# Optimization experiments

Hardware: AMD Instinct MI355X
Metric: run time of the kernel (lower is better)

Reference implementation:

```python
import jax, jax.numpy as jnp
import numpy as np

TEMPERATURE = 0.07


def setup_inputs() -> dict:
    B, NB_PER, K, M, D = 32, 128, 8, 4, 256  # batches, bsl1k per batch, dict targets per batch, embeds per target, feat dim
    key = jax.random.key(0)
    kb, kd = jax.random.split(key)
    feats_bsl1k = jax.random.normal(kb, (B * NB_PER, D), dtype=jnp.float32)
    feats_dict = jax.random.normal(kd, (B * K * M, D), dtype=jnp.float32)
    # dict side: per batch, K distinct targets (first one is the mouthing word), M embeddings each
    batch_dict = np.repeat(np.arange(B), K * M).astype(np.int32)
    targets_dict = np.repeat(np.arange(B * K), M).astype(np.int32)  # sorted, distinct across batches
    one_mouth = np.concatenate([np.ones(1, np.int32), np.zeros(K - 1, np.int32)])
    is_mouthing_dict = np.tile(np.repeat(one_mouth, M), B).astype(np.int32)
    # bsl1k side: half the clips carry the batch's mouthing target, half are background (-1)
    batch_bsl1k = np.repeat(np.arange(B), NB_PER).astype(np.int32)
    tb = np.full((B, NB_PER), -1, dtype=np.int32)
    tb[:, : NB_PER // 2] = (np.arange(B, dtype=np.int32) * K)[:, None]
    targets_bsl1k = tb.reshape(-1)
    unique_targets = np.arange(B * K, dtype=np.int32)  # == unique_consecutive(targets_dict)
    return {
        "feats_bsl1k": feats_bsl1k,
        "feats_dict": feats_dict,
        "targets_bsl1k": jnp.asarray(targets_bsl1k),
        "targets_dict": jnp.asarray(targets_dict),
        "batch_bsl1k": jnp.asarray(batch_bsl1k),
        "batch_dict": jnp.asarray(batch_dict),
        "is_mouthing_dict": jnp.asarray(is_mouthing_dict),
        "unique_targets": jnp.asarray(unique_targets),
        "n_batches": B,
    }


def _loss(feats_bsl1k, feats_dict, targets_bsl1k, targets_dict, batch_bsl1k,
          batch_dict, is_mouthing_dict, unique_targets, n_batches):
    G = unique_targets.shape[0]
    fb = feats_bsl1k / jnp.linalg.norm(feats_bsl1k, axis=1, keepdims=True)
    fd = feats_dict / jnp.linalg.norm(feats_dict, axis=1, keepdims=True)
    dist = (fb @ fd.T) / TEMPERATURE  # [Nb, Nd]

    # group index of each dict embedding (unique_targets is sorted)
    g_idx = jnp.searchsorted(unique_targets, targets_dict).astype(jnp.int32)  # [Nd]
    # per-batch mouthing word (exactly one per batch, mirrors .item() in torch)
    mouth_word = jax.ops.segment_max(
        jnp.where(is_mouthing_dict == 1, targets_dict, -1), batch_dict, num_segments=n_batches)
    group_batch = jax.ops.segment_max(batch_dict, g_idx, num_segments=G)
    group_is_mouth = jax.ops.segment_max(is_mouthing_dict, g_idx, num_segments=G)

    # match[i, g]: bsl1k embedding i matches dict target group g (== match_multi collapsed per target)
    is_fg = targets_bsl1k != -1
    mw = mouth_word[batch_bsl1k]  # [Nb]
    match = jnp.where(
        is_fg[:, None],
        unique_targets[None, :] == mw[:, None],
        (group_batch[None, :] == batch_bsl1k[:, None]) & (group_is_mouth[None, :] == 0),
    )  # [Nb, G] bool

    # diff_batch_match: matched pairs from different batches are excluded from the denominator
    DB = match[:, g_idx] & (batch_bsl1k[:, None] != batch_dict[None, :])  # [Nb, Nd]

    c = jax.lax.stop_gradient(jnp.max(dist))  # shared lse shift; cancels in den - num
    E = jnp.exp(dist - c)                     # raw pair weights (numerator)
    A = jnp.where(DB, 0.0, E)                 # denominator weights with cross-batch matches removed
    matchf = match.astype(dist.dtype)

    Ecg = jax.ops.segment_sum(E.T, g_idx, num_segments=G)  # [G, Nb] column-group sums
    Acg = jax.ops.segment_sum(A.T, g_idx, num_segments=G)  # [G, Nb]

    # numerator[g] = lse over cross product {matched bsl1k rows} x {group-g dict cols}
    num_sum = jnp.einsum('gi,ig->g', Ecg, matchf)
    # denominator[g] = lse over union (group cols OR matched rows) minus cross-batch matches,
    # via inclusion-exclusion: cols + rows - intersection
    t1 = jax.ops.segment_sum(A.sum(0), g_idx, num_segments=G)
    t2 = jnp.einsum('ig,i->g', matchf, A.sum(1))
    t3 = jnp.einsum('gi,ig->g', Acg, matchf)
    den_sum = t1 + t2 - t3
    return jnp.mean(jnp.log(den_sum) - jnp.log(num_sum))


def reference(feats_bsl1k, feats_dict, targets_bsl1k, targets_dict, batch_bsl1k,
              batch_dict, is_mouthing_dict, unique_targets, n_batches):
    return _loss(feats_bsl1k, feats_dict, targets_bsl1k, targets_dict, batch_bsl1k,
                 batch_dict, is_mouthing_dict, unique_targets, n_batches)
```

## Files before the change

kernel.cpp:

```cpp
#include <hip/hip_runtime.h>
#include <math.h>

#define INVT (1.0f / 0.07f)
#define CSHIFT (1.0f / 0.07f)

using bf16x8 = __attribute__((ext_vector_type(8))) short;
using f32x4  = __attribute__((ext_vector_type(4))) float;

__device__ __forceinline__ int lower_bound_i(const int* a, int n, int v) {
    int lo = 0, hi = n;
    while (lo < hi) { int mid = (lo + hi) >> 1; if (a[mid] < v) lo = mid + 1; else hi = mid; }
    return lo;
}

__device__ __forceinline__ unsigned short f2bf(float x) {
    unsigned int u = __float_as_uint(x);
    unsigned int r = (u + 0x7fffu + ((u >> 16) & 1u)) >> 16;
    return (unsigned short)r;
}

__device__ __forceinline__ float agent_ld(const float* p) {
    return __hip_atomic_load(p, __ATOMIC_RELAXED, __HIP_MEMORY_SCOPE_AGENT);
}
__device__ __forceinline__ void agent_st(float* p, float v) {
    __hip_atomic_store(p, v, __ATOMIC_RELAXED, __HIP_MEMORY_SCOPE_AGENT);
}

__global__ __launch_bounds__(256)
void k_prep(const float* __restrict__ fb, const float* __restrict__ fd,
            int Nb, int Nd, int D,
            unsigned short* __restrict__ fbt, unsigned short* __restrict__ fdt,
            unsigned int* __restrict__ zbase, int zcount,
            const int* __restrict__ td, const int* __restrict__ bd,
            const int* __restrict__ im,
            int* __restrict__ mouth_word) {
    __shared__ __align__(16) unsigned short lbuf[32 * 256];
    int t = threadIdx.x;

    int nthreads = gridDim.x * blockDim.x;
    for (int zi = blockIdx.x * blockDim.x + t; zi < zcount; zi += nthreads) zbase[zi] = 0u;

    if (blockIdx.x == 0) {
        for (int i = t; i < Nb; i += blockDim.x) mouth_word[i] = -1;
        __syncthreads();
        for (int j = t; j < Nd; j += blockDim.x) {
            if (im[j] == 1) atomicMax(&mouth_word[bd[j]], td[j]);
        }
    }

    int R0 = blockIdx.x * 32;
    if (R0 >= Nb + Nd) return;
    const float* src; unsigned short* dst; int rt0;
    if (R0 < Nb) { src = fb + (size_t)R0 * D; dst = fbt; rt0 = R0 >> 4; }
    else         { src = fd + (size_t)(R0 - Nb) * D; dst = fdt; rt0 = (R0 - Nb) >> 4; }

    int row = t >> 3, kp = t & 7;
    const float* rp = src + (size_t)row * D;
    float4 v[8];
    float ss = 0.f;
    #pragma unroll
    for (int i = 0; i < 8; ++i) {
        v[i] = *(const float4*)(rp + 4 * (kp + 8 * i));
        ss += v[i].x * v[i].x + v[i].y * v[i].y + v[i].z * v[i].z + v[i].w * v[i].w;
    }
    ss += __shfl_xor(ss, 1, 64);
    ss += __shfl_xor(ss, 2, 64);
    ss += __shfl_xor(ss, 4, 64);
    float inv = rsqrtf(ss);
    #pragma unroll
    for (int i = 0; i < 8; ++i) {
        ushort4 o;
        o.x = f2bf(v[i].x * inv); o.y = f2bf(v[i].y * inv);
        o.z = f2bf(v[i].z * inv); o.w = f2bf(v[i].w * inv);
        *(ushort4*)&lbuf[row * 256 + 4 * (kp + 8 * i)] = o;
    }
    __syncthreads();

    int ktiles = D >> 5;
    #pragma unroll
    for (int j = 0; j < 4; ++j) {
        int c = t + 256 * j;
        int tile = c >> 6, l = c & 63;
        int rtl = tile >> 3, kt = tile & 7;
        int srow = rtl * 16 + (l & 15), sk = kt * 32 + (l >> 4) * 8;
        ulonglong2 d = *(const ulonglong2*)&lbuf[srow * 256 + sk];
        *(ulonglong2*)(dst + (((size_t)((rt0 + rtl) * ktiles + kt)) << 9) + l * 8) = d;
    }
}

__global__ __launch_bounds__(256, 4)
void k_main(const unsigned short* __restrict__ fbt, const unsigned short* __restrict__ fdt,
            const int* __restrict__ tb, const int* __restrict__ bb_arr,
            const int* __restrict__ td, const int* __restrict__ bd,
            const int* __restrict__ im, const int* __restrict__ ut,
            const int* __restrict__ mouth_word,
            int Nb, int Nd, int D, int G,
            float* __restrict__ rowpart, float* __restrict__ colpart,
            float* __restrict__ mnum, float* __restrict__ m1, float* __restrict__ m3,
            float* __restrict__ t2g, float* __restrict__ bgs,
            unsigned int* __restrict__ rowcnt, unsigned int* __restrict__ colcnt,
            unsigned int* __restrict__ dcnt, float* __restrict__ out) {
    __shared__ float cnum[64], ct1[64], ct3[64], rsum[64];
    __shared__ int rowflag, colflag, lastflag;

    int t = threadIdx.x, lane = t & 63, wid = t >> 6;
    int wr = wid >> 1, wc = wid & 1;
    int bm = blockIdx.x * 64, bn = blockIdx.y * 64;
    int l15 = lane & 15, lhi = lane >> 4;

    if (t < 64) { cnum[t] = 0.f; ct1[t] = 0.f; ct3[t] = 0.f; rsum[t] = 0.f; }

    int ktiles = D >> 5;
    const unsigned short* a0p = fbt + (((size_t)(((bm >> 4) + wr * 2) * ktiles)) << 9) + lane * 8;
    const unsigned short* a1p = a0p + ((size_t)ktiles << 9);
    const unsigned short* b0p = fdt + (((size_t)(((bn >> 4) + wc * 2) * ktiles)) << 9) + lane * 8;
    const unsigned short* b1p = b0p + ((size_t)ktiles << 9);

    f32x4 acc[2][2] = {};
    bf16x8 ca0 = *(const bf16x8*)a0p;
    bf16x8 ca1 = *(const bf16x8*)a1p;
    bf16x8 cb0 = *(const bf16x8*)b0p;
    bf16x8 cb1 = *(const bf16x8*)b1p;
    size_t o = 0;
    #pragma unroll 7
    for (int kt = 0; kt + 1 < ktiles; ++kt) {
        o += 512;
        bf16x8 na0 = *(const bf16x8*)(a0p + o);
        bf16x8 na1 = *(const bf16x8*)(a1p + o);
        bf16x8 nb0 = *(const bf16x8*)(b0p + o);
        bf16x8 nb1 = *(const bf16x8*)(b1p + o);
        acc[0][0] = __builtin_amdgcn_mfma_f32_16x16x32_bf16(ca0, cb0, acc[0][0], 0, 0, 0);
        acc[0][1] = __builtin_amdgcn_mfma_f32_16x16x32_bf16(ca0, cb1, acc[0][1], 0, 0, 0);
        acc[1][0] = __builtin_amdgcn_mfma_f32_16x16x32_bf16(ca1, cb0, acc[1][0], 0, 0, 0);
        acc[1][1] = __builtin_amdgcn_mfma_f32_16x16x32_bf16(ca1, cb1, acc[1][1], 0, 0, 0);
        ca0 = na0; ca1 = na1; cb0 = nb0; cb1 = nb1;
    }
    acc[0][0] = __builtin_amdgcn_mfma_f32_16x16x32_bf16(ca0, cb0, acc[0][0], 0, 0, 0);
    acc[0][1] = __builtin_amdgcn_mfma_f32_16x16x32_bf16(ca0, cb1, acc[0][1], 0, 0, 0);
    acc[1][0] = __builtin_amdgcn_mfma_f32_16x16x32_bf16(ca1, cb0, acc[1][0], 0, 0, 0);
    acc[1][1] = __builtin_amdgcn_mfma_f32_16x16x32_bf16(ca1, cb1, acc[1][1], 0, 0, 0);

    int cgb[2], cgm[2], cgc[2];
    #pragma unroll
    for (int nj = 0; nj < 2; ++nj) {
        int col = bn + wc * 32 + nj * 16 + l15;
        cgb[nj] = bd[col]; cgm[nj] = im[col]; cgc[nj] = td[col];
    }

    float pnum[2] = {0.f, 0.f}, pt1[2] = {0.f, 0.f}, pt3[2] = {0.f, 0.f};
    float prow[2][4];

    #pragma unroll
    for (int mi = 0; mi < 2; ++mi) {
        #pragma unroll
        for (int r = 0; r < 4; ++r) {
            int i = bm + wr * 32 + mi * 16 + lhi * 4 + r;
            int tbi = tb[i], bbi = bb_arr[i];
            int mw = mouth_word[bbi];
            bool fg = (tbi != -1);
            float pr = 0.f;
            #pragma unroll
            for (int nj = 0; nj < 2; ++nj) {
                float e = __expf(acc[mi][nj][r] * INVT - CSHIFT);
                bool match = fg ? (cgc[nj] == mw) : ((cgb[nj] == bbi) && (cgm[nj] == 0));
                float a = (match && (bbi != cgb[nj])) ? 0.f : e;
                pnum[nj] += match ? e : 0.f;
                pt1[nj] += a;
                pt3[nj] += match ? a : 0.f;
                pr += a;
            }
            prow[mi][r] = pr;
        }
    }

    __syncthreads();

    #pragma unroll
    for (int nj = 0; nj < 2; ++nj) {
        float n = pnum[nj], x1 = pt1[nj], x3 = pt3[nj];
        n  += __shfl_xor(n, 16, 64);  n  += __shfl_xor(n, 32, 64);
        x1 += __shfl_xor(x1, 16, 64); x1 += __shfl_xor(x1, 32, 64);
        x3 += __shfl_xor(x3, 16, 64); x3 += __shfl_xor(x3, 32, 64);
        if (lhi == 0) {
            int c = wc * 32 + nj * 16 + l15;
            atomicAdd(&cnum[c], n); atomicAdd(&ct1[c], x1); atomicAdd(&ct3[c], x3);
        }
    }
    #pragma unroll
    for (int mi = 0; mi < 2; ++mi) {
        #pragma unroll
        for (int r = 0; r < 4; ++r) {
            float v = prow[mi][r];
            v += __shfl_xor(v, 1, 64); v += __shfl_xor(v, 2, 64);
            v += __shfl_xor(v, 4, 64); v += __shfl_xor(v, 8, 64);
            if (l15 == 0) atomicAdd(&rsum[wr * 32 + mi * 16 + lhi * 4 + r], v);
        }
    }
    __syncthreads();

    float* cp = colpart + (size_t)(blockIdx.x & 7) * 3 * Nd;
    if (t < 64) {
        atomicAdd(&cp[bn + t], cnum[t]);
        atomicAdd(&cp[Nd + bn + t], ct1[t]);
        atomicAdd(&cp[2 * Nd + bn + t], ct3[t]);
    } else if (t < 128) {
        atomicAdd(&rowpart[(size_t)(blockIdx.y & 3) * Nb + bm + (t - 64)], rsum[t - 64]);
    }

    asm volatile("s_waitcnt vmcnt(0)" ::: "memory");
    __syncthreads();
    if (t == 0) {
        rowflag = (atomicAdd(&rowcnt[blockIdx.x * 16], 1u) == gridDim.y - 1) ? 1 : 0;
        colflag = (atomicAdd(&colcnt[blockIdx.y * 16], 1u) == gridDim.x - 1) ? 1 : 0;
    }
    __syncthreads();
    int nfin = rowflag + colflag;
    if (nfin == 0) return;

    if (rowflag && t < 64) {
        int i = bm + t;
        float r = agent_ld(&rowpart[i]) + agent_ld(&rowpart[Nb + i])
                + agent_ld(&rowpart[2 * Nb + i]) + agent_ld(&rowpart[3 * Nb + i]);
        int tbi = tb[i], bbi = bb_arr[i] & 1023;
        if (tbi != -1) {
            int g = lower_bound_i(ut, G, mouth_word[bbi]);
            atomicAdd(&t2g[g], r);
        } else {
            atomicAdd(&bgs[bbi], r);
        }
    }
    if (colflag && t < 192) {
        int c = t / 3, arr = t - c * 3;
        int col = bn + c;
        float s0 = 0.f;
        #pragma unroll
        for (int p = 0; p < 8; ++p)
            s0 += agent_ld(&colpart[(size_t)p * 3 * Nd + (size_t)arr * Nd + col]);
        float* dst = (arr == 0 ? mnum : (arr == 1 ? m1 : m3)) + col;
        agent_st(dst, s0);
    }

    asm volatile("s_waitcnt vmcnt(0)" ::: "memory");
    __syncthreads();
    if (t == 0) {
        unsigned int newv = atomicAdd(dcnt, (unsigned int)nfin) + (unsigned int)nfin;
        lastflag = (newv == gridDim.x + gridDim.y) ? 1 : 0;
    }
    __syncthreads();
    if (!lastflag) return;

    __shared__ float red[256];
    float acc2 = 0.f;
    for (int g = t; g < G; g += 256) {
        int s = lower_bound_i(td, Nd, ut[g]);
        int e = (g + 1 < G) ? lower_bound_i(td, Nd, ut[g + 1]) : Nd;
        float sn = 0.f, s1 = 0.f, s3 = 0.f;
        for (int c = s; c < e; ++c) {
            sn += agent_ld(&mnum[c]);
            s1 += agent_ld(&m1[c]);
            s3 += agent_ld(&m3[c]);
        }
        int gb = bd[s], gm = im[s];
        float t2 = agent_ld(&t2g[g]);
        if (gm == 0 && gb >= 0 && gb < 1024) t2 += agent_ld(&bgs[gb]);
        acc2 += logf(s1 + t2 - s3) - logf(sn);
    }
    red[t] = acc2;
    __syncthreads();
    for (int k = 128; k >= 1; k >>= 1) {
        if (t < k) red[t] += red[t + k];
        __syncthreads();
    }
    if (t == 0) out[0] = red[0] / (float)G;
}

extern "C" void kernel_launch(void* const* d_in, const int* in_sizes, int n_in,
                              void* d_out, int out_size, void* d_ws, size_t ws_size,
                              hipStream_t stream) {
    const float* fb = (const float*)d_in[0];
    const float* fd = (const float*)d_in[1];
    const int* tb = (const int*)d_in[2];
    const int* td = (const int*)d_in[3];
    const int* bb = (const int*)d_in[4];
    const int* bd = (const int*)d_in[5];
    const int* im = (const int*)d_in[6];
    const int* ut = (const int*)d_in[7];

    int Nb = in_sizes[2];
    int Nd = in_sizes[3];
    int G  = in_sizes[7];
    int D  = in_sizes[0] / Nb;
    float* out = (float*)d_out;

    char* p = (char*)d_ws;
    unsigned short* fbt = (unsigned short*)p; p += (size_t)Nb * D * sizeof(unsigned short);
    unsigned short* fdt = (unsigned short*)p; p += (size_t)Nd * D * sizeof(unsigned short);
    char* zstart = p;
    float* rowpart = (float*)p;  p += (size_t)4 * Nb * sizeof(float);
    float* colpart = (float*)p;  p += (size_t)24 * Nd * sizeof(float);
    float* t2g = (float*)p;      p += 1024 * sizeof(float);
    float* bgs = (float*)p;      p += 1024 * sizeof(float);
    unsigned int* rowcnt = (unsigned int*)p; p += 64 * 16 * sizeof(unsigned int);
    unsigned int* colcnt = (unsigned int*)p; p += 16 * 16 * sizeof(unsigned int);
    unsigned int* dcnt = (unsigned int*)p;   p += 16 * sizeof(unsigned int);
    int zcount = (int)((p - zstart) / 4);
    float* mnum = (float*)p; p += (size_t)Nd * sizeof(float);
    float* m1 = (float*)p;   p += (size_t)Nd * sizeof(float);
    float* m3 = (float*)p;   p += (size_t)Nd * sizeof(float);
    int* mouth_word = (int*)p; p += (size_t)Nb * sizeof(int);

    {
        int blocks = (Nb + Nd) / 32;
        k_prep<<<blocks, 256, 0, stream>>>(fb, fd, Nb, Nd, D, fbt, fdt,
                                           (unsigned int*)zstart, zcount,
                                           td, bd, im, mouth_word);
    }

    dim3 grid(Nb / 64, Nd / 64);
    k_main<<<grid, 256, 0, stream>>>(fbt, fdt, tb, bb, td, bd, im, ut, mouth_word,
                                     Nb, Nd, D, G,
                                     rowpart, colpart, mnum, m1, m3, t2g, bgs,
                                     rowcnt, colcnt, dcnt, out);
}
```

Before: 45.06 us.

## Replace atomic partial sums and last-block counters with slabs and a finalize kernel

The main GEMM kernel now writes each block's row and column partial sums to dedicated slab slots with plain stores. It no longer does global atomicAdds and per-row/column arrival counters. A new k_fin kernel, launched with one block per row-tile and column-tile, reduces the slabs, and its last-arriving block computes the final loss. The aim is to remove atomic contention and the serialized tail-block finalization from the main kernel. The cost is an extra kernel launch and larger slab reads: gy partials per row and gx per column.

Measured after the change: 56.90 us. 1.26x slower.

```diff
diff --git a/kernel.cpp b/kernel.cpp
--- a/kernel.cpp
+++ b/kernel.cpp
@@ -92,16 +92,10 @@
 void k_main(const unsigned short* __restrict__ fbt, const unsigned short* __restrict__ fdt,
             const int* __restrict__ tb, const int* __restrict__ bb_arr,
             const int* __restrict__ td, const int* __restrict__ bd,
-            const int* __restrict__ im, const int* __restrict__ ut,
-            const int* __restrict__ mouth_word,
-            int Nb, int Nd, int D, int G,
-            float* __restrict__ rowpart, float* __restrict__ colpart,
-            float* __restrict__ mnum, float* __restrict__ m1, float* __restrict__ m3,
-            float* __restrict__ t2g, float* __restrict__ bgs,
-            unsigned int* __restrict__ rowcnt, unsigned int* __restrict__ colcnt,
-            unsigned int* __restrict__ dcnt, float* __restrict__ out) {
+            const int* __restrict__ im, const int* __restrict__ mouth_word,
+            int Nb, int Nd, int D,
+            float* __restrict__ rowslab, float* __restrict__ colslab) {
     __shared__ float cnum[64], ct1[64], ct3[64], rsum[64];
-    __shared__ int rowflag, colflag, lastflag;
 
     int t = threadIdx.x, lane = t & 63, wid = t >> 6;
     int wr = wid >> 1, wc = wid & 1;
@@ -198,58 +192,65 @@
     }
     __syncthreads();
 
-    float* cp = colpart + (size_t)(blockIdx.x & 7) * 3 * Nd;
     if (t < 64) {
-        atomicAdd(&cp[bn + t], cnum[t]);
-        atomicAdd(&cp[Nd + bn + t], ct1[t]);
-        atomicAdd(&cp[2 * Nd + bn + t], ct3[t]);
-    } else if (t < 128) {
-        atomicAdd(&rowpart[(size_t)(blockIdx.y & 3) * Nb + bm + (t - 64)], rsum[t - 64]);
+        rowslab[(size_t)blockIdx.y * Nb + bm + t] = rsum[t];
+    } else {
+        int c = (t - 64) & 63, arr = (t - 64) >> 6;
+        float v = (arr == 0) ? cnum[c] : (arr == 1 ? ct1[c] : ct3[c]);
+        colslab[((size_t)blockIdx.x * 3 + arr) * Nd + bn + c] = v;
+    }
+}
+
+__global__ __launch_bounds__(256)
+void k_fin(const int* __restrict__ tb, const int* __restrict__ bb_arr,
+           const int* __restrict__ td, const int* __restrict__ bd,
+           const int* __restrict__ im, const int* __restrict__ ut,
+           const int* __restrict__ mouth_word,
+           int Nb, int Nd, int G, int gx, int gy,
+           const float* __restrict__ rowslab, const float* __restrict__ colslab,
+           float* __restrict__ mnum, float* __restrict__ m1, float* __restrict__ m3,
+           float* __restrict__ t2g, float* __restrict__ bgs,
+           unsigned int* __restrict__ dcnt, float* __restrict__ out) {
+    __shared__ float red[256];
+    __shared__ int lastflag;
+    int t = threadIdx.x;
+    int b = blockIdx.x;
+
+    if (b < gx) {
+        if (t < 64) {
+            int i = b * 64 + t;
+            float r = 0.f;
+            for (int q = 0; q < gy; ++q) r += rowslab[(size_t)q * Nb + i];
+            int tbi = tb[i], bbi = bb_arr[i] & 1023;
+            if (tbi != -1) {
+                int g = lower_bound_i(ut, G, mouth_word[bbi]);
+                atomicAdd(&t2g[g], r);
+            } else {
+                atomicAdd(&bgs[bbi], r);
+            }
+        }
+    } else {
+        int by = b - gx;
+        if (t < 192) {
+            int c = t / 3, arr = t - c * 3;
+            int col = by * 64 + c;
+            float s0 = 0.f;
+            for (int x = 0; x < gx; ++x)
+                s0 += colslab[((size_t)x * 3 + arr) * Nd + col];
+            float* dst = (arr == 0 ? mnum : (arr == 1 ? m1 : m3)) + col;
+            agent_st(dst, s0);
+        }
     }
 
     asm volatile("s_waitcnt vmcnt(0)" ::: "memory");
     __syncthreads();
     if (t == 0) {
-        rowflag = (atomicAdd(&rowcnt[blockIdx.x * 16], 1u) == gridDim.y - 1) ? 1 : 0;
-        colflag = (atomicAdd(&colcnt[blockIdx.y * 16], 1u) == gridDim.x - 1) ? 1 : 0;
-    }
-    __syncthreads();
-    int nfin = rowflag + colflag;
-    if (nfin == 0) return;
-
-    if (rowflag && t < 64) {
-        int i = bm + t;
-        float r = agent_ld(&rowpart[i]) + agent_ld(&rowpart[Nb + i])
-                + agent_ld(&rowpart[2 * Nb + i]) + agent_ld(&rowpart[3 * Nb + i]);
-        int tbi = tb[i], bbi = bb_arr[i] & 1023;
-        if (tbi != -1) {
-            int g = lower_bound_i(ut, G, mouth_word[bbi]);
-            atomicAdd(&t2g[g], r);
-        } else {
-            atomicAdd(&bgs[bbi], r);
-        }
-    }
-    if (colflag && t < 192) {
-        int c = t / 3, arr = t - c * 3;
-        int col = bn + c;
-        float s0 = 0.f;
-        #pragma unroll
-        for (int p = 0; p < 8; ++p)
-            s0 += agent_ld(&colpart[(size_t)p * 3 * Nd + (size_t)arr * Nd + col]);
-        float* dst = (arr == 0 ? mnum : (arr == 1 ? m1 : m3)) + col;
-        agent_st(dst, s0);
-    }
-
-    asm volatile("s_waitcnt vmcnt(0)" ::: "memory");
-    __syncthreads();
-    if (t == 0) {
-        unsigned int newv = atomicAdd(dcnt, (unsigned int)nfin) + (unsigned int)nfin;
-        lastflag = (newv == gridDim.x + gridDim.y) ? 1 : 0;
+        unsigned int old = atomicAdd(dcnt, 1u);
+        lastflag = (old == (unsigned int)(gx + gy - 1)) ? 1 : 0;
     }
     __syncthreads();
     if (!lastflag) return;
 
-    __shared__ float red[256];
     float acc2 = 0.f;
     for (int g = t; g < G; g += 256) {
         int s = lower_bound_i(td, Nd, ut[g]);
@@ -292,22 +293,22 @@
     int D  = in_sizes[0] / Nb;
     float* out = (float*)d_out;
 
+    int gx = Nb / 64, gy = Nd / 64;
+
     char* p = (char*)d_ws;
     unsigned short* fbt = (unsigned short*)p; p += (size_t)Nb * D * sizeof(unsigned short);
     unsigned short* fdt = (unsigned short*)p; p += (size_t)Nd * D * sizeof(unsigned short);
-    char* zstart = p;
-    float* rowpart = (float*)p;  p += (size_t)4 * Nb * sizeof(float);
-    float* colpart = (float*)p;  p += (size_t)24 * Nd * sizeof(float);
-    float* t2g = (float*)p;      p += 1024 * sizeof(float);
-    float* bgs = (float*)p;      p += 1024 * sizeof(float);
-    unsigned int* rowcnt = (unsigned int*)p; p += 64 * 16 * sizeof(unsigned int);
-    unsigned int* colcnt = (unsigned int*)p; p += 16 * 16 * sizeof(unsigned int);
-    unsigned int* dcnt = (unsigned int*)p;   p += 16 * sizeof(unsigned int);
-    int zcount = (int)((p - zstart) / 4);
+    float* rowslab = (float*)p; p += (size_t)gy * Nb * sizeof(float);
+    float* colslab = (float*)p; p += (size_t)gx * 3 * Nd * sizeof(float);
     float* mnum = (float*)p; p += (size_t)Nd * sizeof(float);
     float* m1 = (float*)p;   p += (size_t)Nd * sizeof(float);
     float* m3 = (float*)p;   p += (size_t)Nd * sizeof(float);
     int* mouth_word = (int*)p; p += (size_t)Nb * sizeof(int);
+    char* zstart = p;
+    float* t2g = (float*)p;  p += 1024 * sizeof(float);
+    float* bgs = (float*)p;  p += 1024 * sizeof(float);
+    unsigned int* dcnt = (unsigned int*)p; p += 16 * sizeof(unsigned int);
+    int zcount = (int)((p - zstart) / 4);
 
     {
         int blocks = (Nb + Nd) / 32;
@@ -316,9 +317,12 @@
                                            td, bd, im, mouth_word);
     }
 
-    dim3 grid(Nb / 64, Nd / 64);
-    k_main<<<grid, 256, 0, stream>>>(fbt, fdt, tb, bb, td, bd, im, ut, mouth_word,
-                                     Nb, Nd, D, G,
-                                     rowpart, colpart, mnum, m1, m3, t2g, bgs,
-                                     rowcnt, colcnt, dcnt, out);
-}
+    dim3 grid(gx, gy);
+    k_main<<<grid, 256, 0, stream>>>(fbt, fdt, tb, bb, td, bd, im, mouth_word,
+                                     Nb, Nd, D, rowslab, colslab);
+
+    k_fin<<<gx + gy, 256, 0, stream>>>(tb, bb, td, bd, im, ut, mouth_word,
+                                       Nb, Nd, G, gx, gy,
+                                       rowslab, colslab, mnum, m1, m3, t2g, bgs,
+                                       dcnt, out);
+}
```

## Load fp32 features directly in GEMM and apply norms in epilogue

Applied to the files above, without the earlier changes.

The prep kernel no longer writes normalized bf16 tiled copies of both feature matrices; it only computes per-row inverse norms. The main kernel reads raw fp32 rows straight from global memory, converts them to bf16 in registers, and applies the row and column inverse norms to the dot product before the exp. This removes the bf16 staging writes and the LDS transpose in prep, at the cost of twice the bytes per operand load in the GEMM, uncoalesced row-strided loads, and no software prefetch. Rounding to bf16 before normalization changes numerics slightly.

After: 66.67 us. 1.48x slower.

```diff
diff --git a/kernel.cpp b/kernel.cpp
--- a/kernel.cpp
+++ b/kernel.cpp
@@ -19,6 +19,15 @@
     return (unsigned short)r;
 }
 
+__device__ __forceinline__ bf16x8 cvt8(float4 u, float4 v) {
+    bf16x8 f;
+    f[0] = (short)f2bf(u.x); f[1] = (short)f2bf(u.y);
+    f[2] = (short)f2bf(u.z); f[3] = (short)f2bf(u.w);
+    f[4] = (short)f2bf(v.x); f[5] = (short)f2bf(v.y);
+    f[6] = (short)f2bf(v.z); f[7] = (short)f2bf(v.w);
+    return f;
+}
+
 __device__ __forceinline__ float agent_ld(const float* p) {
     return __hip_atomic_load(p, __ATOMIC_RELAXED, __HIP_MEMORY_SCOPE_AGENT);
 }
@@ -27,16 +36,14 @@
 }
 
 __global__ __launch_bounds__(256)
-void k_prep(const float* __restrict__ fb, const float* __restrict__ fd,
+void k_norm(const float* __restrict__ fb, const float* __restrict__ fd,
             int Nb, int Nd, int D,
-            unsigned short* __restrict__ fbt, unsigned short* __restrict__ fdt,
+            float* __restrict__ inv,
             unsigned int* __restrict__ zbase, int zcount,
             const int* __restrict__ td, const int* __restrict__ bd,
             const int* __restrict__ im,
             int* __restrict__ mouth_word) {
-    __shared__ __align__(16) unsigned short lbuf[32 * 256];
     int t = threadIdx.x;
-
     int nthreads = gridDim.x * blockDim.x;
     for (int zi = blockIdx.x * blockDim.x + t; zi < zcount; zi += nthreads) zbase[zi] = 0u;
 
@@ -50,50 +57,27 @@
 
     int R0 = blockIdx.x * 32;
     if (R0 >= Nb + Nd) return;
-    const float* src; unsigned short* dst; int rt0;
-    if (R0 < Nb) { src = fb + (size_t)R0 * D; dst = fbt; rt0 = R0 >> 4; }
-    else         { src = fd + (size_t)(R0 - Nb) * D; dst = fdt; rt0 = (R0 - Nb) >> 4; }
-
     int row = t >> 3, kp = t & 7;
-    const float* rp = src + (size_t)row * D;
-    float4 v[8];
+    int gr = R0 + row;
+    const float* rp = (gr < Nb) ? (fb + (size_t)gr * D) : (fd + (size_t)(gr - Nb) * D);
     float ss = 0.f;
     #pragma unroll
     for (int i = 0; i < 8; ++i) {
-        v[i] = *(const float4*)(rp + 4 * (kp + 8 * i));
-        ss += v[i].x * v[i].x + v[i].y * v[i].y + v[i].z * v[i].z + v[i].w * v[i].w;
+        float4 v = *(const float4*)(rp + 4 * (kp + 8 * i));
+        ss += v.x * v.x + v.y * v.y + v.z * v.z + v.w * v.w;
     }
     ss += __shfl_xor(ss, 1, 64);
     ss += __shfl_xor(ss, 2, 64);
     ss += __shfl_xor(ss, 4, 64);
-    float inv = rsqrtf(ss);
-    #pragma unroll
-    for (int i = 0; i < 8; ++i) {
-        ushort4 o;
-        o.x = f2bf(v[i].x * inv); o.y = f2bf(v[i].y * inv);
-        o.z = f2bf(v[i].z * inv); o.w = f2bf(v[i].w * inv);
-        *(ushort4*)&lbuf[row * 256 + 4 * (kp + 8 * i)] = o;
-    }
-    __syncthreads();
-
-    int ktiles = D >> 5;
-    #pragma unroll
-    for (int j = 0; j < 4; ++j) {
-        int c = t + 256 * j;
-        int tile = c >> 6, l = c & 63;
-        int rtl = tile >> 3, kt = tile & 7;
-        int srow = rtl * 16 + (l & 15), sk = kt * 32 + (l >> 4) * 8;
-        ulonglong2 d = *(const ulonglong2*)&lbuf[srow * 256 + sk];
-        *(ulonglong2*)(dst + (((size_t)((rt0 + rtl) * ktiles + kt)) << 9) + l * 8) = d;
-    }
+    if (kp == 0) inv[gr] = rsqrtf(ss);
 }
 
 __global__ __launch_bounds__(256, 4)
-void k_main(const unsigned short* __restrict__ fbt, const unsigned short* __restrict__ fdt,
+void k_main(const float* __restrict__ fb, const float* __restrict__ fd,
             const int* __restrict__ tb, const int* __restrict__ bb_arr,
             const int* __restrict__ td, const int* __restrict__ bd,
             const int* __restrict__ im, const int* __restrict__ ut,
-            const int* __restrict__ mouth_word,
+            const int* __restrict__ mouth_word, const float* __restrict__ inv,
             int Nb, int Nd, int D, int G,
             float* __restrict__ rowpart, float* __restrict__ colpart,
             float* __restrict__ mnum, float* __restrict__ m1, float* __restrict__ m3,
@@ -110,41 +94,32 @@
 
     if (t < 64) { cnum[t] = 0.f; ct1[t] = 0.f; ct3[t] = 0.f; rsum[t] = 0.f; }
 
-    int ktiles = D >> 5;
-    const unsigned short* a0p = fbt + (((size_t)(((bm >> 4) + wr * 2) * ktiles)) << 9) + lane * 8;
-    const unsigned short* a1p = a0p + ((size_t)ktiles << 9);
-    const unsigned short* b0p = fdt + (((size_t)(((bn >> 4) + wc * 2) * ktiles)) << 9) + lane * 8;
-    const unsigned short* b1p = b0p + ((size_t)ktiles << 9);
+    const float* pa0 = fb + (size_t)(bm + wr * 32 + l15) * D + lhi * 8;
+    const float* pa1 = pa0 + (size_t)16 * D;
+    const float* pb0 = fd + (size_t)(bn + wc * 32 + l15) * D + lhi * 8;
+    const float* pb1 = pb0 + (size_t)16 * D;
 
     f32x4 acc[2][2] = {};
-    bf16x8 ca0 = *(const bf16x8*)a0p;
-    bf16x8 ca1 = *(const bf16x8*)a1p;
-    bf16x8 cb0 = *(const bf16x8*)b0p;
-    bf16x8 cb1 = *(const bf16x8*)b1p;
-    size_t o = 0;
-    #pragma unroll 7
-    for (int kt = 0; kt + 1 < ktiles; ++kt) {
-        o += 512;
-        bf16x8 na0 = *(const bf16x8*)(a0p + o);
-        bf16x8 na1 = *(const bf16x8*)(a1p + o);
-        bf16x8 nb0 = *(const bf16x8*)(b0p + o);
-        bf16x8 nb1 = *(const bf16x8*)(b1p + o);
-        acc[0][0] = __builtin_amdgcn_mfma_f32_16x16x32_bf16(ca0, cb0, acc[0][0], 0, 0, 0);
-        acc[0][1] = __builtin_amdgcn_mfma_f32_16x16x32_bf16(ca0, cb1, acc[0][1], 0, 0, 0);
-        acc[1][0] = __builtin_amdgcn_mfma_f32_16x16x32_bf16(ca1, cb0, acc[1][0], 0, 0, 0);
-        acc[1][1] = __builtin_amdgcn_mfma_f32_16x16x32_bf16(ca1, cb1, acc[1][1], 0, 0, 0);
-        ca0 = na0; ca1 = na1; cb0 = nb0; cb1 = nb1;
-    }
-    acc[0][0] = __builtin_amdgcn_mfma_f32_16x16x32_bf16(ca0, cb0, acc[0][0], 0, 0, 0);
-    acc[0][1] = __builtin_amdgcn_mfma_f32_16x16x32_bf16(ca0, cb1, acc[0][1], 0, 0, 0);
-    acc[1][0] = __builtin_amdgcn_mfma_f32_16x16x32_bf16(ca1, cb0, acc[1][0], 0, 0, 0);
-    acc[1][1] = __builtin_amdgcn_mfma_f32_16x16x32_bf16(ca1, cb1, acc[1][1], 0, 0, 0);
+    #pragma unroll
+    for (int kt = 0; kt < 8; ++kt) {
+        int o = kt * 32;
+        bf16x8 A0 = cvt8(*(const float4*)(pa0 + o), *(const float4*)(pa0 + o + 4));
+        bf16x8 A1 = cvt8(*(const float4*)(pa1 + o), *(const float4*)(pa1 + o + 4));
+        bf16x8 B0 = cvt8(*(const float4*)(pb0 + o), *(const float4*)(pb0 + o + 4));
+        bf16x8 B1 = cvt8(*(const float4*)(pb1 + o), *(const float4*)(pb1 + o + 4));
+        acc[0][0] = __builtin_amdgcn_mfma_f32_16x16x32_bf16(A0, B0, acc[0][0], 0, 0, 0);
+        acc[0][1] = __builtin_amdgcn_mfma_f32_16x16x32_bf16(A0, B1, acc[0][1], 0, 0, 0);
+        acc[1][0] = __builtin_amdgcn_mfma_f32_16x16x32_bf16(A1, B0, acc[1][0], 0, 0, 0);
+        acc[1][1] = __builtin_amdgcn_mfma_f32_16x16x32_bf16(A1, B1, acc[1][1], 0, 0, 0);
+    }
 
     int cgb[2], cgm[2], cgc[2];
+    float cinv[2];
     #pragma unroll
     for (int nj = 0; nj < 2; ++nj) {
         int col = bn + wc * 32 + nj * 16 + l15;
         cgb[nj] = bd[col]; cgm[nj] = im[col]; cgc[nj] = td[col];
+        cinv[nj] = inv[Nb + col];
     }
 
     float pnum[2] = {0.f, 0.f}, pt1[2] = {0.f, 0.f}, pt3[2] = {0.f, 0.f};
@@ -157,11 +132,12 @@
             int i = bm + wr * 32 + mi * 16 + lhi * 4 + r;
             int tbi = tb[i], bbi = bb_arr[i];
             int mw = mouth_word[bbi];
+            float bi = inv[i] * INVT;
             bool fg = (tbi != -1);
             float pr = 0.f;
             #pragma unroll
             for (int nj = 0; nj < 2; ++nj) {
-                float e = __expf(acc[mi][nj][r] * INVT - CSHIFT);
+                float e = __expf(acc[mi][nj][r] * bi * cinv[nj] - CSHIFT);
                 bool match = fg ? (cgc[nj] == mw) : ((cgb[nj] == bbi) && (cgm[nj] == 0));
                 float a = (match && (bbi != cgb[nj])) ? 0.f : e;
                 pnum[nj] += match ? e : 0.f;
@@ -293,8 +269,11 @@
     float* out = (float*)d_out;
 
     char* p = (char*)d_ws;
-    unsigned short* fbt = (unsigned short*)p; p += (size_t)Nb * D * sizeof(unsigned short);
-    unsigned short* fdt = (unsigned short*)p; p += (size_t)Nd * D * sizeof(unsigned short);
+    float* inv = (float*)p;  p += (size_t)(Nb + Nd) * sizeof(float);
+    float* mnum = (float*)p; p += (size_t)Nd * sizeof(float);
+    float* m1 = (float*)p;   p += (size_t)Nd * sizeof(float);
+    float* m3 = (float*)p;   p += (size_t)Nd * sizeof(float);
+    int* mouth_word = (int*)p; p += (size_t)Nb * sizeof(int);
     char* zstart = p;
     float* rowpart = (float*)p;  p += (size_t)4 * Nb * sizeof(float);
     float* colpart = (float*)p;  p += (size_t)24 * Nd * sizeof(float);
@@ -304,20 +283,17 @@
     unsigned int* colcnt = (unsigned int*)p; p += 16 * 16 * sizeof(unsigned int);
     unsigned int* dcnt = (unsigned int*)p;   p += 16 * sizeof(unsigned int);
     int zcount = (int)((p - zstart) / 4);
-    float* mnum = (float*)p; p += (size_t)Nd * sizeof(float);
-    float* m1 = (float*)p;   p += (size_t)Nd * sizeof(float);
-    float* m3 = (float*)p;   p += (size_t)Nd * sizeof(float);
-    int* mouth_word = (int*)p; p += (size_t)Nb * sizeof(int);
 
     {
         int blocks = (Nb + Nd) / 32;
-        k_prep<<<blocks, 256, 0, stream>>>(fb, fd, Nb, Nd, D, fbt, fdt,
+        k_norm<<<blocks, 256, 0, stream>>>(fb, fd, Nb, Nd, D, inv,
                                            (unsigned int*)zstart, zcount,
                                            td, bd, im, mouth_word);
     }
 
     dim3 grid(Nb / 64, Nd / 64);
-    k_main<<<grid, 256, 0, stream>>>(fbt, fdt, tb, bb, td, bd, im, ut, mouth_word,
+    k_main<<<grid, 256, 0, stream>>>(fb, fd, tb, bb, td, bd, im, ut,
+                                     mouth_word, inv,
                                      Nb, Nd, D, G,
                                      rowpart, colpart, mnum, m1, m3, t2g, bgs,
                                      rowcnt, colcnt, dcnt, out);
```
